# Optimization experiments

Measured on AMD Instinct MI355X. Metric: run time of the kernel, lower is better.

## Reference

```python
import jax, jax.numpy as jnp
import numpy as np

NEG = -1e9

def symmetric_quantize(x, bits=8):
    qmax = 2 ** (bits - 1) - 1
    scale = jnp.max(jnp.abs(x)) / qmax
    xq = jnp.clip(jnp.round(x / scale), -(qmax + 1), qmax)
    return xq * scale

def setup_inputs() -> dict:
    key = jax.random.key(0)
    k1, k2, k3, k4, k5 = jax.random.split(key, 5)
    B, S, D = 2, 2048, 1024
    hidden_states = jax.random.normal(k1, (B, S, D), dtype=jnp.float32)
    # additive causal mask [1,1,S,S]
    causal = jnp.tril(jnp.ones((S, S), dtype=bool))
    attention_mask = jnp.where(causal, 0.0, NEG).astype(jnp.float32)[None, None]
    # weights stored (out,in) as used by F.linear; pre-quantized at init (weight_bits=8)
    W_attn = symmetric_quantize(jax.random.normal(k2, (3 * D, D), dtype=jnp.float32) * 0.02)
    b_attn = jax.random.normal(k3, (3 * D,), dtype=jnp.float32) * 0.02
    W_proj = symmetric_quantize(jax.random.normal(k4, (D, D), dtype=jnp.float32) * 0.02)
    b_proj = jax.random.normal(k5, (D,), dtype=jnp.float32) * 0.02
    return {"hidden_states": hidden_states, "attention_mask": attention_mask,
            "W_attn": W_attn, "b_attn": b_attn, "W_proj": W_proj, "b_proj": b_proj}

def reference(hidden_states, attention_mask, W_attn, b_attn, W_proj, b_proj):
    B, S, D = hidden_states.shape
    H = 16
    hd = D // H
    scale = 1.0 / jnp.sqrt(jnp.float32(hd))
    qkv = jnp.einsum('bsd,ed->bse', hidden_states, W_attn) + b_attn  # [B,S,3D]
    q, k, v = jnp.split(qkv, 3, axis=-1)
    def split_heads(x):
        return x.reshape(B, S, H, hd).transpose(0, 2, 1, 3)  # [B,H,S,hd]
    q, k, v = split_heads(q), split_heads(k), split_heads(v)
    # KV-cache fake quant (kv_bits=8)
    k = symmetric_quantize(k)
    v = symmetric_quantize(v)
    present = (k, v)
    scores = jnp.einsum('bhqd,bhkd->bhqk', q, k) * scale + attention_mask
    probs = jax.nn.softmax(scores, axis=-1)  # dropout is identity in eval
    out = jnp.einsum('bhqk,bhkd->bhqd', probs, v)
    out = out.transpose(0, 2, 1, 3).reshape(B, S, D)
    out = symmetric_quantize(out)  # activation fake quant (act_bits=8)
    out = jnp.einsum('bsd,ed->bse', out, W_proj) + b_proj
    return (out, present)
```

## Files before the change

kernel.cpp:

```cpp
#include <hip/hip_runtime.h>
#include <stdint.h>


typedef __attribute__((ext_vector_type(8))) short short8;
typedef __attribute__((ext_vector_type(4))) float floatx4;

#define SSCALE 0.18033688011112042f
#define MASKVAL -30000.0f

__device__ __forceinline__ float bf2f(uint16_t s) {
  return __uint_as_float(((uint32_t)s) << 16);
}
__device__ __forceinline__ uint16_t f2bf(float f) {
  uint32_t u = __float_as_uint(f);
  u += 0x7fffu + ((u >> 16) & 1u);
  return (uint16_t)(u >> 16);
}
__device__ __forceinline__ uint64_t pack4(float a, float b, float c, float d) {
  return (uint64_t)f2bf(a) | ((uint64_t)f2bf(b) << 16) | ((uint64_t)f2bf(c) << 32) |
         ((uint64_t)f2bf(d) << 48);
}
__device__ __forceinline__ float quantize(float v, float inv, float scale) {
  return fminf(fmaxf(rintf(v * inv), -128.f), 127.f) * scale;
}
__device__ __forceinline__ void async_cp16(const void* g, void* l) {
  __builtin_amdgcn_global_load_lds((const __attribute__((address_space(1))) void*)g,
                                   (__attribute__((address_space(3))) void*)l, 16, 0, 0);
}
__device__ __forceinline__ int swz(int row, int bcol) {
  return (row * 128 + bcol) ^ ((row & 7) << 4);
}

__global__ void cvt_kernel(const float* __restrict__ hs, const float* __restrict__ wa,
                           const float* __restrict__ wp, uint16_t* __restrict__ hs_b,
                           uint16_t* __restrict__ wa_b, uint16_t* __restrict__ wp_b) {
  const size_t qi = (size_t)blockIdx.x * 256 + threadIdx.x;
  const float* src;
  uint16_t* dst;
  size_t off;
  if (qi < 1048576) {
    src = hs; dst = hs_b; off = qi;
  } else if (qi < 1835008) {
    src = wa; dst = wa_b; off = qi - 1048576;
  } else {
    src = wp; dst = wp_b; off = qi - 1835008;
  }
  const float4 f = ((const float4*)src)[off];
  ((uint64_t*)dst)[off] = pack4(f.x, f.y, f.z, f.w);
}

__global__ __launch_bounds__(256) void gemm_qkv(const uint16_t* __restrict__ A,
                                                const uint16_t* __restrict__ W,
                                                const float* __restrict__ bias,
                                                uint16_t* __restrict__ q_ws,
                                                float* __restrict__ kd,
                                                float* __restrict__ vd,
                                                float* __restrict__ scal) {
  __shared__ uint16_t a_sh[2][128 * 32];
  __shared__ uint16_t b_sh[2][128 * 32];
  __shared__ float wred[4];
  const int tid = threadIdx.x;
  const int lane = tid & 63, wid = tid >> 6;
  const int quad = lane >> 4, l16 = lane & 15;
  const int m0 = blockIdx.y * 128, n0 = blockIdx.x * 128;
  const int wrow = (wid >> 1) * 64, wcol = (wid & 1) * 64;
  const uint16_t* Ab = A + (size_t)m0 * 1024;
  const uint16_t* Wb = W + (size_t)n0 * 1024;

  floatx4 acc[4][4] = {};

  auto stage = [&](int buf, int k0) {
#pragma unroll
    for (int i = 0; i < 2; ++i) {
      const int chunk = tid + 256 * i;
      async_cp16(Ab + (size_t)(chunk >> 2) * 1024 + k0 + (chunk & 3) * 8,
                 (char*)a_sh[buf] + (size_t)(wid * 64 + 256 * i) * 16);
      async_cp16(Wb + (size_t)(chunk >> 2) * 1024 + k0 + (chunk & 3) * 8,
                 (char*)b_sh[buf] + (size_t)(wid * 64 + 256 * i) * 16);
    }
  };

  stage(0, 0);
  __syncthreads();
  int cur = 0;
  for (int k0 = 0; k0 < 1024; k0 += 32) {
    if (k0 + 32 < 1024) stage(cur ^ 1, k0 + 32);
    short8 af[4], bfr[4];
#pragma unroll
    for (int mi = 0; mi < 4; ++mi)
      af[mi] = *(const short8*)&a_sh[cur][(wrow + mi * 16 + l16) * 32 + quad * 8];
#pragma unroll
    for (int ni = 0; ni < 4; ++ni)
      bfr[ni] = *(const short8*)&b_sh[cur][(wcol + ni * 16 + l16) * 32 + quad * 8];
#pragma unroll
    for (int mi = 0; mi < 4; ++mi)
#pragma unroll
      for (int ni = 0; ni < 4; ++ni)
        acc[mi][ni] =
            __builtin_amdgcn_mfma_f32_16x16x32_bf16(af[mi], bfr[ni], acc[mi][ni], 0, 0, 0);
    __syncthreads();
    cur ^= 1;
  }

  const int cat = n0 >> 10;
  float tmax = 0.f;
#pragma unroll
  for (int mi = 0; mi < 4; ++mi) {
#pragma unroll
    for (int ni = 0; ni < 4; ++ni) {
      const int col = n0 + wcol + ni * 16 + l16;
      const float bv = bias[col];
#pragma unroll
      for (int r = 0; r < 4; ++r) {
        const int row = m0 + wrow + mi * 16 + quad * 4 + r;
        const float v = acc[mi][ni][r] + bv;
        if (cat == 0) {
          q_ws[(size_t)row * 1024 + col] = f2bf(v * SSCALE);
        } else {
          const int cc = col & 1023, h = cc >> 6, dd = cc & 63;
          const int b = row >> 11, s = row & 2047;
          float* dst = (cat == 1) ? kd : vd;
          dst[(((size_t)b * 16 + h) * 2048 + s) * 64 + dd] = v;
          tmax = fmaxf(tmax, fabsf(v));
        }
      }
    }
  }
  if (cat > 0) {
#pragma unroll
    for (int off = 32; off; off >>= 1) tmax = fmaxf(tmax, __shfl_xor(tmax, off));
    if (lane == 0) wred[wid] = tmax;
    __syncthreads();
    if (tid == 0) {
      const float m = fmaxf(fmaxf(wred[0], wred[1]), fmaxf(wred[2], wred[3]));
      atomicMax((unsigned int*)(scal + (cat - 1)), __float_as_uint(m));
    }
  }
}

__global__ void quant_kv(float* __restrict__ kd, float* __restrict__ vd,
                         const float* __restrict__ scal, uint16_t* __restrict__ kc,
                         uint16_t* __restrict__ vt) {
  __shared__ uint16_t tile[64 * 65];
  const int t = blockIdx.z, bh = blockIdx.y, s0 = blockIdx.x * 64;
  const float mx = t ? scal[1] : scal[0];
  const float scale = mx / 127.f;
  const float inv = (mx > 0.f) ? 127.f / mx : 0.f;
  float* base = (t ? vd : kd) + ((size_t)bh * 2048 + s0) * 64;
  const int tid = threadIdx.x;
#pragma unroll
  for (int i = 0; i < 16; ++i) {
    const int e = tid + 256 * i;
    const float q = quantize(base[e], inv, scale);
    base[e] = q;
    if (t)
      tile[(e >> 6) * 65 + (e & 63)] = f2bf(q);
    else
      kc[((size_t)bh * 2048 + s0) * 64 + e] = f2bf(q);
  }
  if (t) {
    __syncthreads();
#pragma unroll
    for (int i = 0; i < 16; ++i) {
      const int e = tid + 256 * i;
      const int dd = e >> 6, sr = e & 63;
      vt[((size_t)bh * 64 + dd) * 2048 + s0 + sr] = tile[sr * 65 + dd];
    }
  }
}

__global__ __launch_bounds__(512) void attn_kernel(const uint16_t* __restrict__ q_ws,
                                                   const uint16_t* __restrict__ kc,
                                                   const uint16_t* __restrict__ vt,
                                                   uint16_t* __restrict__ at,
                                                   float* __restrict__ omax) {
  __shared__ uint16_t qp_sh[128 * 64];
  __shared__ uint16_t k_sh[2][64 * 64];
  __shared__ uint16_t v_sh[2][64 * 64];
  __shared__ float wred[8];

  const int tid = threadIdx.x, lane = tid & 63, wid = tid >> 6;
  const int quad = lane >> 4, l16 = lane & 15;
  const int qt = (blockIdx.y & 16) ? (int)blockIdx.x : (15 - (int)blockIdx.x);
  const int bh = blockIdx.y;
  const int b = bh >> 4, h = bh & 15;
  const int wq0 = wid * 16;
  const int sr = tid >> 3, sc8 = (tid & 7) * 8;
  const uint16_t* kbase = kc + (size_t)bh * 131072;
  const uint16_t* vtbase = vt + (size_t)bh * 131072;

  const int q0 = qt * 128;
  const int jmax = 2 * qt + 1;
  const int base = q0 + wq0;
  const int rowg = base + l16;

  uint4 kr = *(const uint4*)&kbase[tid * 8];
  uint4 vr = *(const uint4*)&vtbase[(size_t)sr * 2048 + sc8];

#pragma unroll
  for (int i = 0; i < 2; ++i) {
    const int idx = tid + 512 * i;
    const int r = idx >> 3, c8 = (idx & 7) * 8;
    *(uint4*)((char*)qp_sh + swz(r, c8 * 2)) =
        *(const uint4*)&q_ws[(size_t)(b * 2048 + q0 + r) * 1024 + h * 64 + c8];
  }
  *(uint4*)((char*)k_sh[0] + swz(sr, sc8 * 2)) = kr;
  *(uint4*)((char*)v_sh[0] + swz(sr, sc8 * 2)) = vr;
  __syncthreads();

  short8 qa[2];
#pragma unroll
  for (int ks = 0; ks < 2; ++ks)
    qa[ks] = *(const short8*)((const char*)qp_sh + swz(wq0 + l16, ks * 64 + quad * 16));

  const int pr = wq0 + l16;

  floatx4 o[4] = {};
  float mst = MASKVAL, lst = 0.f;

  for (int j = 0; j <= jmax; ++j) {
    const int cur = j & 1;
    uint4 krn, vrn;
    if (j < jmax) {
      krn = *(const uint4*)&kbase[(size_t)(j + 1) * 4096 + tid * 8];
      vrn = *(const uint4*)&vtbase[(size_t)sr * 2048 + (j + 1) * 64 + sc8];
    }
    __builtin_amdgcn_sched_barrier(0);

    const int jb = j * 64;
    if (jb <= base + 15) {
      floatx4 s[4] = {};
#pragma unroll
      for (int ks = 0; ks < 2; ++ks) {
        short8 kf[4];
#pragma unroll
        for (int ni = 0; ni < 4; ++ni)
          kf[ni] = *(const short8*)((const char*)k_sh[cur] +
                                    swz(ni * 16 + l16, ks * 64 + quad * 16));
#pragma unroll
        for (int ni = 0; ni < 4; ++ni)
          s[ni] = __builtin_amdgcn_mfma_f32_16x16x32_bf16(kf[ni], qa[ks], s[ni], 0, 0, 0);
      }

      if (jb + 63 > base) {
#pragma unroll
        for (int ni = 0; ni < 4; ++ni)
#pragma unroll
          for (int r = 0; r < 4; ++r)
            if (jb + ni * 16 + quad * 4 + r > rowg) s[ni][r] = MASKVAL;
      }
      float rmax = MASKVAL;
#pragma unroll
      for (int ni = 0; ni < 4; ++ni)
#pragma unroll
        for (int r = 0; r < 4; ++r) rmax = fmaxf(rmax, s[ni][r]);
      rmax = fmaxf(rmax, __shfl_xor(rmax, 16));
      rmax = fmaxf(rmax, __shfl_xor(rmax, 32));

      if (__any(rmax > mst + 8.f)) {
        const float mnew = fmaxf(mst, rmax);
        const float a = exp2f(mst - mnew);
        lst *= a;
#pragma unroll
        for (int ni = 0; ni < 4; ++ni)
#pragma unroll
          for (int r = 0; r < 4; ++r) o[ni][r] *= a;
        mst = mnew;
      }

#pragma unroll
      for (int ni = 0; ni < 4; ++ni) {
        const float e0 = exp2f(s[ni][0] - mst);
        const float e1 = exp2f(s[ni][1] - mst);
        const float e2 = exp2f(s[ni][2] - mst);
        const float e3 = exp2f(s[ni][3] - mst);
        lst += (e0 + e1) + (e2 + e3);
        uint32_t w0, w1;
        asm("v_cvt_pk_bf16_f32 %0, %1, %2" : "=v"(w0) : "v"(e0), "v"(e1));
        asm("v_cvt_pk_bf16_f32 %0, %1, %2" : "=v"(w1) : "v"(e2), "v"(e3));
        uint2 pw;
        pw.x = w0;
        pw.y = w1;
        *(uint2*)((char*)qp_sh + swz(pr, ni * 32 + quad * 8)) = pw;
      }

#pragma unroll
      for (int ks = 0; ks < 2; ++ks) {
        const short8 pb = *(const short8*)((const char*)qp_sh + swz(pr, ks * 64 + quad * 16));
        short8 vf[4];
#pragma unroll
        for (int ni = 0; ni < 4; ++ni)
          vf[ni] = *(const short8*)((const char*)v_sh[cur] +
                                    swz(ni * 16 + l16, ks * 64 + quad * 16));
#pragma unroll
        for (int ni = 0; ni < 4; ++ni)
          o[ni] = __builtin_amdgcn_mfma_f32_16x16x32_bf16(vf[ni], pb, o[ni], 0, 0, 0);
      }
    }

    if (j < jmax) {
      *(uint4*)((char*)k_sh[1 - cur] + swz(sr, sc8 * 2)) = krn;
      *(uint4*)((char*)v_sh[1 - cur] + swz(sr, sc8 * 2)) = vrn;
    }
    __syncthreads();
  }

  float l = lst;
  l += __shfl_xor(l, 16);
  l += __shfl_xor(l, 32);
  const float invl = 1.f / fmaxf(l, 1e-30f);
  const size_t rowoff = (size_t)(b * 2048 + rowg) * 1024 + h * 64;
  float tmax = 0.f;
#pragma unroll
  for (int ni = 0; ni < 4; ++ni) {
    const float v0 = o[ni][0] * invl;
    const float v1 = o[ni][1] * invl;
    const float v2 = o[ni][2] * invl;
    const float v3 = o[ni][3] * invl;
    tmax = fmaxf(tmax, fmaxf(fmaxf(fabsf(v0), fabsf(v1)), fmaxf(fabsf(v2), fabsf(v3))));
    *(uint64_t*)&at[rowoff + ni * 16 + quad * 4] = pack4(v0, v1, v2, v3);
  }

#pragma unroll
  for (int off = 32; off; off >>= 1) tmax = fmaxf(tmax, __shfl_xor(tmax, off));
  if (lane == 0) wred[wid] = tmax;
  __syncthreads();
  if (tid == 0) {
    float m = wred[0];
#pragma unroll
    for (int i = 1; i < 8; ++i) m = fmaxf(m, wred[i]);
    atomicMax((unsigned int*)omax, __float_as_uint(m));
  }
}

__global__ void quant_act(uint16_t* __restrict__ a, const float* __restrict__ omax) {
  const size_t i = ((size_t)blockIdx.x * 256 + threadIdx.x) * 8;
  const float mx = *omax;
  const float scale = mx / 127.f;
  const float inv = (mx > 0.f) ? 127.f / mx : 0.f;
  uint16_t v[8];
  *(uint4*)v = *(const uint4*)&a[i];
#pragma unroll
  for (int k = 0; k < 8; ++k) v[k] = f2bf(quantize(bf2f(v[k]), inv, scale));
  *(uint4*)&a[i] = *(const uint4*)v;
}

__global__ __launch_bounds__(256) void gemm_proj(const uint16_t* __restrict__ A,
                                                 const uint16_t* __restrict__ W,
                                                 const float* __restrict__ bias,
                                                 float* __restrict__ C) {
  __shared__ uint16_t a_sh[2][128 * 32];
  __shared__ uint16_t b_sh[2][64 * 32];
  const int tid = threadIdx.x;
  const int lane = tid & 63, wid = tid >> 6;
  const int quad = lane >> 4, l16 = lane & 15;
  const int m0 = blockIdx.y * 128, n0 = blockIdx.x * 64;
  const int wrow = (wid >> 1) * 64, wcol = (wid & 1) * 32;
  const uint16_t* Ab = A + (size_t)m0 * 1024;
  const uint16_t* Wb = W + (size_t)n0 * 1024;

  floatx4 acc[4][2] = {};

  auto stage = [&](int buf, int k0) {
#pragma unroll
    for (int i = 0; i < 2; ++i) {
      const int chunk = tid + 256 * i;
      async_cp16(Ab + (size_t)(chunk >> 2) * 1024 + k0 + (chunk & 3) * 8,
                 (char*)a_sh[buf] + (size_t)(wid * 64 + 256 * i) * 16);
    }
    async_cp16(Wb + (size_t)(tid >> 2) * 1024 + k0 + (tid & 3) * 8,
               (char*)b_sh[buf] + (size_t)(wid * 64) * 16);
  };

  stage(0, 0);
  __syncthreads();
  int cur = 0;
  for (int k0 = 0; k0 < 1024; k0 += 32) {
    if (k0 + 32 < 1024) stage(cur ^ 1, k0 + 32);
    short8 af[4], bfr[2];
#pragma unroll
    for (int mi = 0; mi < 4; ++mi)
      af[mi] = *(const short8*)&a_sh[cur][(wrow + mi * 16 + l16) * 32 + quad * 8];
#pragma unroll
    for (int ni = 0; ni < 2; ++ni)
      bfr[ni] = *(const short8*)&b_sh[cur][(wcol + ni * 16 + l16) * 32 + quad * 8];
#pragma unroll
    for (int mi = 0; mi < 4; ++mi)
#pragma unroll
      for (int ni = 0; ni < 2; ++ni)
        acc[mi][ni] =
            __builtin_amdgcn_mfma_f32_16x16x32_bf16(af[mi], bfr[ni], acc[mi][ni], 0, 0, 0);
    __syncthreads();
    cur ^= 1;
  }

#pragma unroll
  for (int mi = 0; mi < 4; ++mi) {
#pragma unroll
    for (int ni = 0; ni < 2; ++ni) {
      const int col = n0 + wcol + ni * 16 + l16;
      const float bv = bias[col];
#pragma unroll
      for (int r = 0; r < 4; ++r) {
        const int row = m0 + wrow + mi * 16 + quad * 4 + r;
        C[(size_t)row * 1024 + col] = acc[mi][ni][r] + bv;
      }
    }
  }
}

extern "C" void kernel_launch(void* const* d_in, const int* in_sizes, int n_in,
                              void* d_out, int out_size, void* d_ws, size_t ws_size,
                              hipStream_t stream) {
  const float* hs = (const float*)d_in[0];
  const float* Wa = (const float*)d_in[2];
  const float* ba = (const float*)d_in[3];
  const float* Wp = (const float*)d_in[4];
  const float* bp = (const float*)d_in[5];

  float* outd = (float*)d_out;
  float* kd = outd + (size_t)4194304;
  float* vd = outd + (size_t)8388608;

  char* ws = (char*)d_ws;
  const size_t MB = 1024 * 1024;
  uint16_t* hs_b = (uint16_t*)ws;
  uint16_t* Wa_b = (uint16_t*)(ws + 8 * MB);
  uint16_t* Wp_b = (uint16_t*)(ws + 14 * MB);
  uint16_t* q_ws = (uint16_t*)(ws + 16 * MB);
  uint16_t* kc = (uint16_t*)(ws + 24 * MB);
  uint16_t* vt = (uint16_t*)(ws + 32 * MB);
  uint16_t* at = (uint16_t*)(ws + 40 * MB);
  float* scal = (float*)(ws + 48 * MB);

  hipMemsetAsync(scal, 0, 4 * sizeof(float), stream);
  cvt_kernel<<<8192, 256, 0, stream>>>(hs, Wa, Wp, hs_b, Wa_b, Wp_b);
  gemm_qkv<<<dim3(24, 32), 256, 0, stream>>>(hs_b, Wa_b, ba, q_ws, kd, vd, scal);
  quant_kv<<<dim3(32, 32, 2), 256, 0, stream>>>(kd, vd, scal, kc, vt);
  attn_kernel<<<dim3(16, 32), 512, 0, stream>>>(q_ws, kc, vt, at, scal + 2);
  quant_act<<<2048, 256, 0, stream>>>(at, scal + 2);
  gemm_proj<<<dim3(16, 32), 256, 0, stream>>>(at, Wp_b, bp, outd);
}
```

Baseline: 226.8 us.

## Triple-buffer LDS staging in QKV and projection GEMMs with one barrier per step

Both GEMM kernels go from double-buffered to triple-buffered shared-memory staging. Async copies are issued two k-steps ahead, and a partial vmcnt wait plus a single barrier per iteration replaces the end-of-loop __syncthreads. The aim is to hide global load latency and cut one sync per k-step. In exchange, LDS use per block rises by 50%, which may reduce occupancy, and correctness depends on the hand-counted vmcnt values matching the copy instructions actually issued per stage.

Measured after the change: 222.0 us. 2.1% less time.

```diff
diff --git a/kernel.cpp b/kernel.cpp
--- a/kernel.cpp
+++ b/kernel.cpp
@@ -56,8 +56,8 @@
                                                 float* __restrict__ kd,
                                                 float* __restrict__ vd,
                                                 float* __restrict__ scal) {
-  __shared__ uint16_t a_sh[2][128 * 32];
-  __shared__ uint16_t b_sh[2][128 * 32];
+  __shared__ uint16_t a_sh[3][128 * 32];
+  __shared__ uint16_t b_sh[3][128 * 32];
   __shared__ float wred[4];
   const int tid = threadIdx.x;
   const int lane = tid & 63, wid = tid >> 6;
@@ -80,11 +80,7 @@
     }
   };
 
-  stage(0, 0);
-  __syncthreads();
-  int cur = 0;
-  for (int k0 = 0; k0 < 1024; k0 += 32) {
-    if (k0 + 32 < 1024) stage(cur ^ 1, k0 + 32);
+  auto compute = [&](int cur) {
     short8 af[4], bfr[4];
 #pragma unroll
     for (int mi = 0; mi < 4; ++mi)
@@ -98,9 +94,22 @@
       for (int ni = 0; ni < 4; ++ni)
         acc[mi][ni] =
             __builtin_amdgcn_mfma_f32_16x16x32_bf16(af[mi], bfr[ni], acc[mi][ni], 0, 0, 0);
-    __syncthreads();
-    cur ^= 1;
-  }
+  };
+
+  stage(0, 0);
+  stage(1, 32);
+  for (int k0 = 0; k0 < 992; k0 += 32) {
+    const int cur = (k0 >> 5) % 3;
+    asm volatile("s_waitcnt vmcnt(4)" ::: "memory");
+    __builtin_amdgcn_s_barrier();
+    __builtin_amdgcn_sched_barrier(0);
+    compute(cur);
+    if (k0 <= 928) stage((cur + 2) % 3, k0 + 64);
+  }
+  asm volatile("s_waitcnt vmcnt(0)" ::: "memory");
+  __builtin_amdgcn_s_barrier();
+  __builtin_amdgcn_sched_barrier(0);
+  compute((992 >> 5) % 3);
 
   const int cat = n0 >> 10;
   float tmax = 0.f;
@@ -349,8 +358,8 @@
                                                  const uint16_t* __restrict__ W,
                                                  const float* __restrict__ bias,
                                                  float* __restrict__ C) {
-  __shared__ uint16_t a_sh[2][128 * 32];
-  __shared__ uint16_t b_sh[2][64 * 32];
+  __shared__ uint16_t a_sh[3][128 * 32];
+  __shared__ uint16_t b_sh[3][64 * 32];
   const int tid = threadIdx.x;
   const int lane = tid & 63, wid = tid >> 6;
   const int quad = lane >> 4, l16 = lane & 15;
@@ -372,11 +381,7 @@
                (char*)b_sh[buf] + (size_t)(wid * 64) * 16);
   };
 
-  stage(0, 0);
-  __syncthreads();
-  int cur = 0;
-  for (int k0 = 0; k0 < 1024; k0 += 32) {
-    if (k0 + 32 < 1024) stage(cur ^ 1, k0 + 32);
+  auto compute = [&](int cur) {
     short8 af[4], bfr[2];
 #pragma unroll
     for (int mi = 0; mi < 4; ++mi)
@@ -390,9 +395,22 @@
       for (int ni = 0; ni < 2; ++ni)
         acc[mi][ni] =
             __builtin_amdgcn_mfma_f32_16x16x32_bf16(af[mi], bfr[ni], acc[mi][ni], 0, 0, 0);
-    __syncthreads();
-    cur ^= 1;
-  }
+  };
+
+  stage(0, 0);
+  stage(1, 32);
+  for (int k0 = 0; k0 < 992; k0 += 32) {
+    const int cur = (k0 >> 5) % 3;
+    asm volatile("s_waitcnt vmcnt(3)" ::: "memory");
+    __builtin_amdgcn_s_barrier();
+    __builtin_amdgcn_sched_barrier(0);
+    compute(cur);
+    if (k0 <= 928) stage((cur + 2) % 3, k0 + 64);
+  }
+  asm volatile("s_waitcnt vmcnt(0)" ::: "memory");
+  __builtin_amdgcn_s_barrier();
+  __builtin_amdgcn_sched_barrier(0);
+  compute((992 >> 5) % 3);
 
 #pragma unroll
   for (int mi = 0; mi < 4; ++mi) {
```
